# Kernel tuning notes

Measured on AMD Instinct MI355X. Metric: run time of the kernel, lower is better.

The kernel has to match this reference:

```python
import jax, jax.numpy as jnp
from jax import lax
import numpy as np

T, B, C_IN, H, W = 8, 4, 3, 30, 32
HID = 128
SCALE = 0.02


def _convlstm_layer(x_seq, Wk, b):
    """x_seq: (T,B,Cin,H,W); Wk: (4*HID, Cin+HID, 3, 3); b: (4*HID,).
    Returns (h_seq (T,B,HID,H,W), h_last (B,HID,H,W))."""
    Bb, _, Hh, Ww = x_seq.shape[1], x_seq.shape[2], x_seq.shape[3], x_seq.shape[4]
    h0 = jnp.zeros((x_seq.shape[1], HID, x_seq.shape[3], x_seq.shape[4]), x_seq.dtype)
    c0 = jnp.zeros_like(h0)

    def step(carry, xt):
        h, c = carry
        combined = jnp.concatenate([xt, h], axis=1)  # (B, Cin+HID, H, W)
        conv = lax.conv_general_dilated(
            combined, Wk, window_strides=(1, 1), padding='SAME',
            dimension_numbers=('NCHW', 'OIHW', 'NCHW')) + b[None, :, None, None]
        cc_i, cc_f, cc_o, cc_g = jnp.split(conv, 4, axis=1)
        i = jax.nn.sigmoid(cc_i)
        f = jax.nn.sigmoid(cc_f)
        o = jax.nn.sigmoid(cc_o)
        g = jnp.tanh(cc_g)
        c_next = f * c + i * g
        h_next = o * jnp.tanh(c_next)
        return (h_next, c_next), h_next

    (h_last, _), h_seq = lax.scan(step, (h0, c0), x_seq)
    return h_seq, h_last


def setup_inputs() -> dict:
    key = jax.random.key(0)
    ks = jax.random.split(key, 14)
    x = jax.random.normal(ks[0], (T, B, C_IN, H, W), jnp.float32)
    # layer 0: in = 3 + 128; layers 1-3: in = 128 + 128; out = 4*128 gates
    W0 = jax.random.normal(ks[1], (4 * HID, C_IN + HID, 3, 3), jnp.float32) * SCALE
    b0 = jnp.zeros((4 * HID,), jnp.float32)
    W1 = jax.random.normal(ks[2], (4 * HID, 2 * HID, 3, 3), jnp.float32) * SCALE
    b1 = jnp.zeros((4 * HID,), jnp.float32)
    W2 = jax.random.normal(ks[3], (4 * HID, 2 * HID, 3, 3), jnp.float32) * SCALE
    b2 = jnp.zeros((4 * HID,), jnp.float32)
    W3 = jax.random.normal(ks[4], (4 * HID, 2 * HID, 3, 3), jnp.float32) * SCALE
    b3 = jnp.zeros((4 * HID,), jnp.float32)
    lin1_w = jax.random.normal(ks[5], (256, HID * H * W), jnp.float32) * SCALE
    lin1_b = jnp.zeros((256,), jnp.float32)
    lin2_w = jax.random.normal(ks[6], (2, 256), jnp.float32) * SCALE
    lin2_b = jnp.zeros((2,), jnp.float32)
    return dict(x=x, W0=W0, b0=b0, W1=W1, b1=b1, W2=W2, b2=b2, W3=W3, b3=b3,
                lin1_w=lin1_w, lin1_b=lin1_b, lin2_w=lin2_w, lin2_b=lin2_b)


def reference(x, W0, b0, W1, b1, W2, b2, W3, b3, lin1_w, lin1_b, lin2_w, lin2_b):
    seq = x
    h_last = None
    for Wk, bk in ((W0, b0), (W1, b1), (W2, b2), (W3, b3)):
        seq, h_last = _convlstm_layer(seq, Wk, bk)
    flat = h_last.reshape(h_last.shape[0], -1)  # (B, 128*30*32)
    z = jax.nn.relu(flat @ lin1_w.T + lin1_b) @ lin2_w.T + lin2_b  # (B, 2)
    mu, sigma = z[:, :1], z[:, 1:]
    return mu, sigma
```

## Files before the change

kernel.cpp:

```cpp
#include <hip/hip_runtime.h>
#include <math.h>

#define T_ 8
#define B_ 4
#define CIN_ 3
#define H_ 30
#define W_ 32
#define HID_ 128
#define NPOS_ (H_*W_)
#define CHW_ (HID_*NPOS_)
#define BCHW_ ((size_t)B_*CHW_)
#define LIN1_IN_ (HID_*NPOS_)

#define HS_ROW_ 1088
#define HS_CH_  39168
#define HS_SLOT_ 1253376

typedef __attribute__((ext_vector_type(8))) short bs8;
typedef __attribute__((ext_vector_type(4))) float f32x4;
typedef unsigned int __attribute__((address_space(1))) gas_u32;
typedef unsigned int __attribute__((address_space(3))) las_u32;

__device__ __forceinline__ void gload16(const void* g, void* l) {
  __builtin_amdgcn_global_load_lds((const gas_u32*)g, (las_u32*)l, 16, 0, 0);
}

__device__ __forceinline__ unsigned short f2bf(float f) {
  unsigned u = __float_as_uint(f);
  return (unsigned short)((u + 0x7fffu + ((u >> 16) & 1u)) >> 16);
}
__device__ __forceinline__ float bf2f(unsigned short h) {
  return __uint_as_float(((unsigned)h) << 16);
}
__device__ __forceinline__ void split2(float v, unsigned short& h,
                                       unsigned short& m) {
  h = f2bf(v);
  m = f2bf(v - bf2f(h));
}

__global__ __launch_bounds__(256)
void wsplit(const float* __restrict__ W, unsigned short* __restrict__ Wsp,
            int CTOT, int ci_off, int total)
{
  int i = blockIdx.x * 256 + threadIdx.x;
  if (i >= total) return;
  int ci8 = i & 7;
  int oc  = (i >> 3) & 127;
  int kg  = (i >> 10) & 3;
  int mtl = (i >> 12) & 3;
  int r   = i >> 14;
  int tap = r % 9;
  int ks  = r / 9;
  int ky = tap / 3, kx = tap % 3;
  int g = ks * 3 + ky;
  int ocp = mtl * 128 + oc;
  int hid = ocp >> 2, gate = ocp & 3;
  int cio = ci_off + ks * 32 + kg * 8 + ci8;
  float v = W[((size_t)(gate * HID_ + hid) * CTOT + cio) * 9 + tap];
  int ocs = (oc & 0x70) | ((oc ^ (kg << 1)) & 0x0F);
  Wsp[((size_t)(g * 4 + mtl) * 3 + kx) * 4096 + kg * 1024 + ocs * 8 + ci8]
      = f2bf(v);
}

__global__ __launch_bounds__(256)
void wtx(const float* __restrict__ W0, float* __restrict__ Wxp)
{
  int i = blockIdx.x * 256 + threadIdx.x;
  if (i >= 512 * 27) return;
  int ocp = i / 27, rem = i % 27;
  int ci = rem / 9, tap = rem % 9;
  int hid = ocp >> 2, gate = ocp & 3;
  Wxp[i] = W0[((size_t)(gate * HID_ + hid) * 131 + ci) * 9 + tap];
}

struct StepSlot {
  const unsigned short* Wsp;
  const float* Wxp;
  const unsigned short* xs;
  const unsigned short* hs;
  const float* xraw;
  const float* bias;
  float* hout;
  float* cbuf;
  unsigned short* hsout;
  int nchunk; int is_l0;
};
struct StepArgs { StepSlot s[4]; };

__global__ __launch_bounds__(256, 2)
void conv_mfma(StepArgs args)
{
  const int bx = blockIdx.x;
  const int mt = bx & 3;
  const StepSlot sl = args.s[bx >> 2];
  const int tid = threadIdx.x;
  const int nt = blockIdx.y;
  const int b  = nt / 15;
  const int y0 = (nt % 15) * 2;
  const int lane = tid & 63;
  const int wid = tid >> 6;
  const int wm = wid >> 1;
  const int wn = wid & 1;
  const int lanelo = lane & 15;
  const int kgl = lane >> 4;
  const int lsw = lanelo ^ (kgl << 1);

  __shared__ __align__(16) unsigned short sact[8704];
  __shared__ __align__(16) unsigned short sW[2][12288];

  f32x4 acc[4][2];
  #pragma unroll
  for (int mf = 0; mf < 4; ++mf)
    #pragma unroll
    for (int nf = 0; nf < 2; ++nf)
      acc[mf][nf] = (f32x4){0.f, 0.f, 0.f, 0.f};

  if (sl.is_l0) {
    float* sWx = (float*)&sW[0][0];
    for (int q = tid; q < 128 * 27; q += 256)
      sWx[q] = sl.Wxp[(size_t)mt * 128 * 27 + q];
    __syncthreads();
    const int y = y0 + wn;
    #pragma unroll
    for (int nf = 0; nf < 2; ++nf) {
      const int x = nf * 16 + lanelo;
      float xw[3][3][3];
      #pragma unroll
      for (int ci = 0; ci < 3; ++ci)
        #pragma unroll
        for (int ky = 0; ky < 3; ++ky)
          #pragma unroll
          for (int kx = 0; kx < 3; ++kx) {
            int yy = y + ky - 1, xx = x + kx - 1;
            xw[ci][ky][kx] = ((unsigned)yy < 30u && (unsigned)xx < 32u)
                ? sl.xraw[((size_t)(b * 3 + ci) * H_ + yy) * W_ + xx] : 0.f;
          }
      #pragma unroll
      for (int mf = 0; mf < 4; ++mf)
        #pragma unroll
        for (int g = 0; g < 4; ++g) {
          int oc = wm * 64 + mf * 16 + (kgl << 2) + g;
          float s = 0.f;
          #pragma unroll
          for (int ci = 0; ci < 3; ++ci)
            #pragma unroll
            for (int kk = 0; kk < 9; ++kk)
              s = fmaf(sWx[oc * 27 + ci * 9 + kk], xw[ci][kk / 3][kk % 3], s);
          acc[mf][nf][g] += s;
        }
    }
    __syncthreads();
  }

  const int NCH = sl.nchunk;

  auto stageAct = [&](int c) {
    const unsigned short* src; int ch;
    if (sl.xs) { if (c < 4) { src = sl.xs; ch = c; } else { src = sl.hs; ch = c - 4; } }
    else       { src = sl.hs; ch = c; }
    #pragma unroll
    for (int s = 0; s < 2; ++s) {
      const uint4* g = (const uint4*)(src + (((size_t)b * 2 + s) * 4 + ch) * HS_CH_
                                      + (size_t)y0 * HS_ROW_);
      uint4* d = (uint4*)(sact + s * 4352);
      for (int q = tid; q < 544; q += 256) d[q] = g[q];
    }
  };

  auto stageW = [&](int g, int buf) {
    const char* src = (const char*)(sl.Wsp + (size_t)(g * 4 + mt) * 12288);
    char* d = (char*)&sW[buf][0];
    const int off = tid * 16;
    #pragma unroll
    for (int q = 0; q < 6; ++q)
      gload16(src + off + q * 4096, d + off + q * 4096);
  };

  if (NCH > 0) {
    stageAct(0);
    stageW(0, 0);
    __syncthreads();
    const int NG = NCH * 3;
    int g = 0;
    for (int c = 0; c < NCH; ++c) {
      #pragma unroll
      for (int kyg = 0; kyg < 3; ++kyg, ++g) {
        if (g > 0) {
          asm volatile("s_waitcnt vmcnt(0)");
          __builtin_amdgcn_s_barrier();
          __builtin_amdgcn_sched_barrier(0);
        }
        if (g + 1 < NG)
          stageW(g + 1, (g + 1) & 1);
        const bs8* Bv = (const bs8*)sact;
        const bs8* Aw = (const bs8*)&sW[g & 1][0];
        #pragma unroll
        for (int kx = 0; kx < 3; ++kx) {
          bs8 Bf[2][2];
          #pragma unroll
          for (int s = 0; s < 2; ++s)
            #pragma unroll
            for (int nf = 0; nf < 2; ++nf)
              Bf[s][nf] = Bv[((s * 4 + wn + kyg) * 4 + kgl) * 34
                             + nf * 16 + lanelo + kx];
          bs8 Af[4];
          #pragma unroll
          for (int mf = 0; mf < 4; ++mf)
            Af[mf] = Aw[kx * 512 + kgl * 128 + wm * 64 + mf * 16 + lsw];
          #pragma unroll
          for (int sb = 0; sb < 2; ++sb)
            #pragma unroll
            for (int mf = 0; mf < 4; ++mf)
              #pragma unroll
              for (int nf = 0; nf < 2; ++nf)
                acc[mf][nf] = __builtin_amdgcn_mfma_f32_16x16x32_bf16(
                    Af[mf], Bf[sb][nf], acc[mf][nf], 0, 0, 0);
        }
        __builtin_amdgcn_sched_barrier(0);
      }
      if (c + 1 < NCH) {
        __builtin_amdgcn_s_barrier();
        __builtin_amdgcn_sched_barrier(0);
        stageAct(c + 1);
        __syncthreads();
      }
    }
  }

  float hv[4][2];
  const int y = y0 + wn;
  #pragma unroll
  for (int mf = 0; mf < 4; ++mf) {
    const int hlo = wm * 16 + mf * 4 + kgl;
    const int hid = mt * 32 + hlo;
    const float b0 = sl.bias[hid];
    const float b1 = sl.bias[128 + hid];
    const float b2 = sl.bias[256 + hid];
    const float b3 = sl.bias[384 + hid];
    #pragma unroll
    for (int nf = 0; nf < 2; ++nf) {
      const int x = nf * 16 + lanelo;
      const size_t idx = ((size_t)(b * HID_ + hid) * H_ + y) * W_ + x;
      float vi = acc[mf][nf][0] + b0;
      float vf = acc[mf][nf][1] + b1;
      float vo = acc[mf][nf][2] + b2;
      float vg = acc[mf][nf][3] + b3;
      float ig = 1.f / (1.f + expf(-vi));
      float fg = 1.f / (1.f + expf(-vf));
      float og = 1.f / (1.f + expf(-vo));
      float gg = tanhf(vg);
      float cn = fg * sl.cbuf[idx] + ig * gg;
      sl.cbuf[idx] = cn;
      float hn = og * tanhf(cn);
      if (sl.hout) sl.hout[idx] = hn;
      hv[mf][nf] = hn;
    }
  }

  if (sl.hsout) {
    __syncthreads();
    unsigned short* hl = sact;
    #pragma unroll
    for (int mf = 0; mf < 4; ++mf) {
      const int hlo = wm * 16 + mf * 4 + kgl;
      const int kg = hlo >> 3, cl = hlo & 7;
      #pragma unroll
      for (int nf = 0; nf < 2; ++nf) {
        const int x = nf * 16 + lanelo;
        unsigned short hh, hm;
        split2(hv[mf][nf], hh, hm);
        int o = (wn * 4 + kg) * 256 + x * 8 + cl;
        hl[o] = hh; hl[o + 2048] = hm;
      }
    }
    __syncthreads();
    for (int q = tid; q < 512; q += 256) {
      int s = q >> 8, rem = q & 255;
      int r = rem >> 7, kg = (rem >> 5) & 3, x = rem & 31;
      uint4 v = *(const uint4*)&hl[(((s * 2 + r) * 4 + kg) * 32 + x) * 8];
      unsigned short* dst = sl.hsout
          + ((((size_t)b * 2 + s) * 4 + mt) * 36 + (y0 + r + 1)) * HS_ROW_
          + (kg * 34 + x + 1) * 8;
      *(uint4*)dst = v;
    }
  }
}

__global__ __launch_bounds__(256)
void lin1_part(const float* __restrict__ h, const float* __restrict__ w,
               float* __restrict__ part)
{
  const int bid = blockIdx.x;
  const int o  = bid >> 3;
  const int ks = bid & 7;
  const int tid = threadIdx.x;
  const float4* w4 = (const float4*)(w + (size_t)o * LIN1_IN_) + ks * 3840;
  const float4* h4 = (const float4*)h + ks * 3840;
  float acc[4] = {0.f, 0.f, 0.f, 0.f};
  for (int i = tid; i < 3840; i += 256) {
    float4 wv = w4[i];
    #pragma unroll
    for (int b = 0; b < 4; ++b) {
      float4 hv = h4[(size_t)b * 30720 + i];
      acc[b] = fmaf(wv.x, hv.x, fmaf(wv.y, hv.y,
               fmaf(wv.z, hv.z, fmaf(wv.w, hv.w, acc[b]))));
    }
  }
  #pragma unroll
  for (int b = 0; b < 4; ++b)
    for (int m = 32; m; m >>= 1) acc[b] += __shfl_xor(acc[b], m);
  __shared__ float red[4][4];
  if ((tid & 63) == 0) {
    #pragma unroll
    for (int b = 0; b < 4; ++b) red[tid >> 6][b] = acc[b];
  }
  __syncthreads();
  if (tid == 0) {
    #pragma unroll
    for (int b = 0; b < 4; ++b) {
      float s = red[0][b] + red[1][b] + red[2][b] + red[3][b];
      part[((size_t)b * 256 + o) * 8 + ks] = s;
    }
  }
}

__global__ __launch_bounds__(256)
void lin1_finish(const float* __restrict__ part, const float* __restrict__ bias,
                 float* __restrict__ z1)
{
  int i = blockIdx.x * 256 + threadIdx.x;
  if (i < 1024) {
    int o = i & 255;
    float s = bias[o];
    #pragma unroll
    for (int k = 0; k < 8; ++k) s += part[(size_t)i * 8 + k];
    z1[i] = fmaxf(s, 0.f);
  }
}

__global__ __launch_bounds__(64)
void lin2_kernel(const float* __restrict__ z1, const float* __restrict__ w2,
                 const float* __restrict__ b2, float* __restrict__ out)
{
  const int lane = threadIdx.x;
  for (int p = 0; p < 8; ++p) {
    int j = p >> 2, b = p & 3;
    float acc = 0.f;
    for (int k = lane; k < 256; k += 64)
      acc = fmaf(z1[b * 256 + k], w2[j * 256 + k], acc);
    for (int m = 32; m; m >>= 1) acc += __shfl_xor(acc, m);
    if (lane == 0) out[p] = acc + b2[j];
  }
}

extern "C" void kernel_launch(void* const* d_in, const int* in_sizes, int n_in,
                              void* d_out, int out_size, void* d_ws, size_t ws_size,
                              hipStream_t stream) {
  const float* x = (const float*)d_in[0];
  const float* Wks[4] = {(const float*)d_in[1], (const float*)d_in[3],
                         (const float*)d_in[5], (const float*)d_in[7]};
  const float* bks[4] = {(const float*)d_in[2], (const float*)d_in[4],
                         (const float*)d_in[6], (const float*)d_in[8]};
  const float* lin1_w = (const float*)d_in[9];
  const float* lin1_b = (const float*)d_in[10];
  const float* lin2_w = (const float*)d_in[11];
  const float* lin2_b = (const float*)d_in[12];
  float* out = (float*)d_out;

  const int CTOTs[4] = {131, 256, 256, 256};
  const int NKS[4]   = {4, 8, 8, 8};

  unsigned short* up = (unsigned short*)d_ws;
  unsigned short* wsp[4];
  for (int l = 0; l < 4; ++l) {
    wsp[l] = up;
    up += (size_t)NKS[l] * 9 * 4 * 4096;
  }
  unsigned short* hsr0 = up;
  unsigned short* hsr[4];
  for (int l = 0; l < 4; ++l) { hsr[l] = up; up += 2 * (size_t)HS_SLOT_; }
  float* fp = (float*)up;
  float* wxp = fp;   fp += 512 * 27;
  float* hlast = fp; fp += BCHW_;
  float* cbase = fp; fp += 4 * BCHW_;
  float* part = fp;  fp += 4 * 256 * 8;
  float* z1 = fp;    fp += 1024;

  wtx<<<dim3(54), dim3(256), 0, stream>>>(Wks[0], wxp);
  for (int l = 0; l < 4; ++l) {
    int total = NKS[l] * 9 * 4 * 4096;
    wsplit<<<dim3((total + 255) / 256), dim3(256), 0, stream>>>(
        Wks[l], wsp[l], CTOTs[l], (l == 0) ? 3 : 0, total);
  }
  hipMemsetAsync(cbase, 0, 4 * BCHW_ * sizeof(float), stream);
  hipMemsetAsync(hsr0, 0, 8 * (size_t)HS_SLOT_ * sizeof(unsigned short), stream);

  for (int d = 0; d <= 10; ++d) {
    StepArgs a;
    int n = 0;
    for (int l = 0; l < 4; ++l) {
      int t = d - l;
      if (t < 0 || t > 7) continue;
      StepSlot& s = a.s[n++];
      s.is_l0 = (l == 0);
      s.Wsp = wsp[l];
      s.Wxp = (l == 0) ? wxp : nullptr;
      s.xraw = (l == 0) ? x + (size_t)t * B_ * CIN_ * NPOS_ : nullptr;
      s.xs = (l == 0) ? nullptr : hsr[l - 1] + (size_t)(t & 1) * HS_SLOT_;
      s.hs = (t == 0) ? nullptr : hsr[l] + (size_t)((t - 1) & 1) * HS_SLOT_;
      s.bias = bks[l];
      s.hout = (l == 3 && t == 7) ? hlast : nullptr;
      s.cbuf = cbase + (size_t)l * BCHW_;
      s.hsout = hsr[l] + (size_t)(t & 1) * HS_SLOT_;
      s.nchunk = (l == 0) ? (t ? 4 : 0) : (t ? 8 : 4);
    }
    for (int z = n; z < 4; ++z) a.s[z] = a.s[0];
    conv_mfma<<<dim3(4 * n, 60), dim3(256), 0, stream>>>(a);
  }

  lin1_part<<<dim3(2048), dim3(256), 0, stream>>>(hlast, lin1_w, part);
  lin1_finish<<<dim3(4), dim3(256), 0, stream>>>(part, lin1_b, z1);
  lin2_kernel<<<dim3(1), dim3(64), 0, stream>>>(z1, lin2_w, lin2_b, out);
}
```

Baseline: 1.156 ms.

## Retile ConvLSTM MFMA kernel to 64-channel by 4-row tiles with higher occupancy

The conv_mfma block tile changes from 128 gate outputs × 2 image rows (waves in a 2×2 grid) to 64 gate outputs × 4 rows (all four waves along rows). The weight pre-split layout and the weight staging shrink to match, the activation staging grows to 6 rows, and launch bounds move from 2 to 3 blocks per SM, aiming to cut per-block weight traffic and LDS use and improve occupancy. Since 30 rows do not divide by 4, the last row tile computes two padding rows whose results are masked on store, which is wasted MFMA work. Layer-0 input weights are now held in LDS as bf16 instead of fp32, which slightly lowers precision for that layer.

```diff
diff --git a/kernel.cpp b/kernel.cpp
--- a/kernel.cpp
+++ b/kernel.cpp
@@ -45,20 +45,20 @@
   int i = blockIdx.x * 256 + threadIdx.x;
   if (i >= total) return;
   int ci8 = i & 7;
-  int oc  = (i >> 3) & 127;
-  int kg  = (i >> 10) & 3;
-  int mtl = (i >> 12) & 3;
+  int oc  = (i >> 3) & 63;
+  int kg  = (i >> 9) & 3;
+  int mtl = (i >> 11) & 7;
   int r   = i >> 14;
   int tap = r % 9;
   int ks  = r / 9;
   int ky = tap / 3, kx = tap % 3;
   int g = ks * 3 + ky;
-  int ocp = mtl * 128 + oc;
+  int ocp = mtl * 64 + oc;
   int hid = ocp >> 2, gate = ocp & 3;
   int cio = ci_off + ks * 32 + kg * 8 + ci8;
   float v = W[((size_t)(gate * HID_ + hid) * CTOT + cio) * 9 + tap];
-  int ocs = (oc & 0x70) | ((oc ^ (kg << 1)) & 0x0F);
-  Wsp[((size_t)(g * 4 + mtl) * 3 + kx) * 4096 + kg * 1024 + ocs * 8 + ci8]
+  int ocs = (oc & 0x30) | ((oc ^ (kg << 1)) & 0x0F);
+  Wsp[((size_t)(g * 8 + mtl) * 3 + kx) * 2048 + kg * 512 + ocs * 8 + ci8]
       = f2bf(v);
 }
 
@@ -87,26 +87,24 @@
 };
 struct StepArgs { StepSlot s[4]; };
 
-__global__ __launch_bounds__(256, 2)
+__global__ __launch_bounds__(256, 3)
 void conv_mfma(StepArgs args)
 {
   const int bx = blockIdx.x;
-  const int mt = bx & 3;
-  const StepSlot sl = args.s[bx >> 2];
+  const int mt = bx & 7;
+  const StepSlot sl = args.s[bx >> 3];
   const int tid = threadIdx.x;
   const int nt = blockIdx.y;
-  const int b  = nt / 15;
-  const int y0 = (nt % 15) * 2;
+  const int b  = nt >> 3;
+  const int y0 = (nt & 7) * 4;
   const int lane = tid & 63;
-  const int wid = tid >> 6;
-  const int wm = wid >> 1;
-  const int wn = wid & 1;
+  const int wn = tid >> 6;
   const int lanelo = lane & 15;
   const int kgl = lane >> 4;
   const int lsw = lanelo ^ (kgl << 1);
 
-  __shared__ __align__(16) unsigned short sact[8704];
-  __shared__ __align__(16) unsigned short sW[2][12288];
+  __shared__ __align__(16) unsigned short sact[13056];
+  __shared__ __align__(16) unsigned short sW[2][6144];
 
   f32x4 acc[4][2];
   #pragma unroll
@@ -116,9 +114,9 @@
       acc[mf][nf] = (f32x4){0.f, 0.f, 0.f, 0.f};
 
   if (sl.is_l0) {
-    float* sWx = (float*)&sW[0][0];
-    for (int q = tid; q < 128 * 27; q += 256)
-      sWx[q] = sl.Wxp[(size_t)mt * 128 * 27 + q];
+    unsigned short* sWx = sact;
+    for (int q = tid; q < 64 * 27; q += 256)
+      sWx[q] = f2bf(sl.Wxp[(size_t)mt * 64 * 27 + q]);
     __syncthreads();
     const int y = y0 + wn;
     #pragma unroll
@@ -139,13 +137,14 @@
       for (int mf = 0; mf < 4; ++mf)
         #pragma unroll
         for (int g = 0; g < 4; ++g) {
-          int oc = wm * 64 + mf * 16 + (kgl << 2) + g;
+          int oc = mf * 16 + (kgl << 2) + g;
           float s = 0.f;
           #pragma unroll
           for (int ci = 0; ci < 3; ++ci)
             #pragma unroll
             for (int kk = 0; kk < 9; ++kk)
-              s = fmaf(sWx[oc * 27 + ci * 9 + kk], xw[ci][kk / 3][kk % 3], s);
+              s = fmaf(bf2f(sWx[oc * 27 + ci * 9 + kk]),
+                       xw[ci][kk / 3][kk % 3], s);
           acc[mf][nf][g] += s;
         }
     }
@@ -162,17 +161,17 @@
     for (int s = 0; s < 2; ++s) {
       const uint4* g = (const uint4*)(src + (((size_t)b * 2 + s) * 4 + ch) * HS_CH_
                                       + (size_t)y0 * HS_ROW_);
-      uint4* d = (uint4*)(sact + s * 4352);
-      for (int q = tid; q < 544; q += 256) d[q] = g[q];
+      uint4* d = (uint4*)(sact + s * 6528);
+      for (int q = tid; q < 816; q += 256) d[q] = g[q];
     }
   };
 
   auto stageW = [&](int g, int buf) {
-    const char* src = (const char*)(sl.Wsp + (size_t)(g * 4 + mt) * 12288);
+    const char* src = (const char*)(sl.Wsp + (size_t)(g * 8 + mt) * 6144);
     char* d = (char*)&sW[buf][0];
     const int off = tid * 16;
     #pragma unroll
-    for (int q = 0; q < 6; ++q)
+    for (int q = 0; q < 3; ++q)
       gload16(src + off + q * 4096, d + off + q * 4096);
   };
 
@@ -201,12 +200,12 @@
           for (int s = 0; s < 2; ++s)
             #pragma unroll
             for (int nf = 0; nf < 2; ++nf)
-              Bf[s][nf] = Bv[((s * 4 + wn + kyg) * 4 + kgl) * 34
+              Bf[s][nf] = Bv[((s * 6 + wn + kyg) * 4 + kgl) * 34
                              + nf * 16 + lanelo + kx];
           bs8 Af[4];
           #pragma unroll
           for (int mf = 0; mf < 4; ++mf)
-            Af[mf] = Aw[kx * 512 + kgl * 128 + wm * 64 + mf * 16 + lsw];
+            Af[mf] = Aw[kx * 256 + kgl * 64 + mf * 16 + lsw];
           #pragma unroll
           for (int sb = 0; sb < 2; ++sb)
             #pragma unroll
@@ -229,10 +228,11 @@
 
   float hv[4][2];
   const int y = y0 + wn;
+  const bool valid = (y < 30);
   #pragma unroll
   for (int mf = 0; mf < 4; ++mf) {
-    const int hlo = wm * 16 + mf * 4 + kgl;
-    const int hid = mt * 32 + hlo;
+    const int hlo = mf * 4 + kgl;
+    const int hid = mt * 16 + hlo;
     const float b0 = sl.bias[hid];
     const float b1 = sl.bias[128 + hid];
     const float b2 = sl.bias[256 + hid];
@@ -249,10 +249,13 @@
       float fg = 1.f / (1.f + expf(-vf));
       float og = 1.f / (1.f + expf(-vo));
       float gg = tanhf(vg);
-      float cn = fg * sl.cbuf[idx] + ig * gg;
-      sl.cbuf[idx] = cn;
+      float cprev = valid ? sl.cbuf[idx] : 0.f;
+      float cn = fg * cprev + ig * gg;
       float hn = og * tanhf(cn);
-      if (sl.hout) sl.hout[idx] = hn;
+      if (valid) {
+        sl.cbuf[idx] = cn;
+        if (sl.hout) sl.hout[idx] = hn;
+      }
       hv[mf][nf] = hn;
     }
   }
@@ -262,26 +265,30 @@
     unsigned short* hl = sact;
     #pragma unroll
     for (int mf = 0; mf < 4; ++mf) {
-      const int hlo = wm * 16 + mf * 4 + kgl;
-      const int kg = hlo >> 3, cl = hlo & 7;
+      const int hlo = mf * 4 + kgl;
+      const int kgloc = hlo >> 3, cl = hlo & 7;
       #pragma unroll
       for (int nf = 0; nf < 2; ++nf) {
         const int x = nf * 16 + lanelo;
         unsigned short hh, hm;
         split2(hv[mf][nf], hh, hm);
-        int o = (wn * 4 + kg) * 256 + x * 8 + cl;
+        int o = (((0 * 4 + wn) * 2 + kgloc) * 32 + x) * 8 + cl;
         hl[o] = hh; hl[o + 2048] = hm;
       }
     }
     __syncthreads();
+    const int ch = mt >> 1;
+    const int kgbase = (mt & 1) * 2;
     for (int q = tid; q < 512; q += 256) {
-      int s = q >> 8, rem = q & 255;
-      int r = rem >> 7, kg = (rem >> 5) & 3, x = rem & 31;
-      uint4 v = *(const uint4*)&hl[(((s * 2 + r) * 4 + kg) * 32 + x) * 8];
-      unsigned short* dst = sl.hsout
-          + ((((size_t)b * 2 + s) * 4 + mt) * 36 + (y0 + r + 1)) * HS_ROW_
-          + (kg * 34 + x + 1) * 8;
-      *(uint4*)dst = v;
+      int x = q & 31, kgloc = (q >> 5) & 1, r = (q >> 6) & 3, s = q >> 8;
+      if (y0 + r < 30) {
+        uint4 v = *(const uint4*)&hl[(((s * 4 + r) * 2 + kgloc) * 32 + x) * 8];
+        unsigned short* dst = sl.hsout
+            + (((size_t)b * 2 + s) * 4 + ch) * HS_CH_
+            + (size_t)(y0 + r + 1) * HS_ROW_
+            + ((kgbase + kgloc) * 34 + x + 1) * 8;
+        *(uint4*)dst = v;
+      }
     }
   }
 }
@@ -415,7 +422,7 @@
       s.nchunk = (l == 0) ? (t ? 4 : 0) : (t ? 8 : 4);
     }
     for (int z = n; z < 4; ++z) a.s[z] = a.s[0];
-    conv_mfma<<<dim3(4 * n, 60), dim3(256), 0, stream>>>(a);
+    conv_mfma<<<dim3(8 * n, 32), dim3(256), 0, stream>>>(a);
   }
 
   lin1_part<<<dim3(2048), dim3(256), 0, stream>>>(hlast, lin1_w, part);
```

Measured after the change: 1.174 ms. About the same (+1.6%).
